# Kernel tuning notes

Hardware: AMD Instinct MI355X
Metric: run time of the kernel (lower is better)

The kernel has to match this reference:

```python
import jax, jax.numpy as jnp
import numpy as np

NUM_HEADS = 16
NUM_HIDDENS = 1024
NEG_INF = -1e6


def setup_inputs() -> dict:
    key = jax.random.key(0)
    ks = jax.random.split(key, 8)
    B, S, D = 2, 2048, NUM_HIDDENS
    scale = 1.0 / np.sqrt(D)
    return {
        "q": jax.random.normal(ks[0], (B, S, D), jnp.float32),
        "k": jax.random.normal(ks[1], (B, S, D), jnp.float32),
        "v": jax.random.normal(ks[2], (B, S, D), jnp.float32),
        # nn.Linear weights have shape (out_features, in_features)
        "Wq": jax.random.normal(ks[3], (D, D), jnp.float32) * scale,
        "Wk": jax.random.normal(ks[4], (D, D), jnp.float32) * scale,
        "Wv": jax.random.normal(ks[5], (D, D), jnp.float32) * scale,
        "Wo": jax.random.normal(ks[6], (D, D), jnp.float32) * scale,
        "valid_len": jax.random.randint(ks[7], (B,), 1, 2048 + 1, jnp.int32),
    }


def _unpack_heads(x, nh):
    # (B, S, H) -> (B*nh, S, H//nh), matching Unpack_base_head
    B, S, H = x.shape
    return x.reshape(B, S, nh, H // nh).transpose(0, 2, 1, 3).reshape(B * nh, S, H // nh)


def _merge_heads(x, nh):
    # Faithful to Merge_base_head: (B*nh, S, dh) -> (B, nh, S, dh)
    # -> permute(0,2,3,1) -> (B, S, dh, nh) -> (B, S, dh*nh)
    Bnh, S, dh = x.shape
    B = Bnh // nh
    x = x.reshape(B, nh, S, dh).transpose(0, 2, 3, 1)
    return x.reshape(B, S, dh * nh)


def reference(q, k, v, Wq, Wk, Wv, Wo, valid_len):
    nh = NUM_HEADS
    # projections (bias=False); Linear: x @ W.T
    qh = _unpack_heads(q @ Wq.T, nh)  # (B*nh, S, dh)
    kh = _unpack_heads(k @ Wk.T, nh)
    vh = _unpack_heads(v @ Wv.T, nh)
    dh = qh.shape[-1]
    scores = jnp.einsum("bqd,bkd->bqk", qh, kh) / jnp.sqrt(jnp.float32(dh))
    # repeat_interleave valid_len by num_heads along dim 0
    vl = jnp.repeat(valid_len, nh)  # (B*nh,)
    key_pos = jnp.arange(scores.shape[-1])  # (S,)
    mask = key_pos[None, None, :] < vl[:, None, None]  # (B*nh, 1, S)
    scores = jnp.where(mask, scores, NEG_INF)
    attn = jax.nn.softmax(scores, axis=-1)  # dropout=0.0 (eval) -> identity
    out = jnp.einsum("bqk,bkd->bqd", attn, vh)  # (B*nh, S, dh)
    out = _merge_heads(out, nh) @ Wo.T  # (B, S, H)
    return out, attn
```

## Files before the change

### kernel.cpp

```cpp
#include <hip/hip_runtime.h>
#include <stdint.h>

#define SB 2048
#define DB 1024
#define NHB 16
#define DHB 64

typedef __attribute__((ext_vector_type(8))) short short8;
typedef __attribute__((ext_vector_type(4))) short short4v;
typedef __attribute__((ext_vector_type(4))) float f32x4;

#define SC2 0.18033688011112042f

__device__ __forceinline__ unsigned short f2bf(float f) {
  union { float f; uint32_t u; } v; v.f = f;
  uint32_t u = v.u;
  return (unsigned short)((u + 0x7FFFu + ((u >> 16) & 1u)) >> 16);
}

__device__ __forceinline__ void gld16(const void* g, void* l) {
  __builtin_amdgcn_global_load_lds(
      (const __attribute__((address_space(1))) void*)g,
      (__attribute__((address_space(3))) void*)l, 16, 0, 0);
}

__device__ __forceinline__ int xcd_swz(int bid, int nwg) {
  return (bid & 7) * (nwg >> 3) + (bid >> 3);
}

struct ConvArgs {
  const float* s[7];
  unsigned short* d[7];
  int n[7];
};

__global__ __launch_bounds__(256) void conv_kernel(ConvArgs a) {
  const int t = blockIdx.y;
  const float* __restrict__ src = a.s[t];
  unsigned short* __restrict__ dst = a.d[t];
  const int n8 = a.n[t] >> 3;
  for (int i = blockIdx.x * 256 + threadIdx.x; i < n8; i += gridDim.x * 256) {
    const f32x4* p = (const f32x4*)src + (size_t)i * 2;
    f32x4 x = p[0], y = p[1];
    short8 o;
    o[0] = (short)f2bf(x[0]); o[1] = (short)f2bf(x[1]);
    o[2] = (short)f2bf(x[2]); o[3] = (short)f2bf(x[3]);
    o[4] = (short)f2bf(y[0]); o[5] = (short)f2bf(y[1]);
    o[6] = (short)f2bf(y[2]); o[7] = (short)f2bf(y[3]);
    *(short8*)(dst + (size_t)i * 8) = o;
  }
}

struct GemmArgs {
  const unsigned short* A[3];
  const unsigned short* B[3];
  void* O[3];
  int mode[3];
};

__global__ __launch_bounds__(256) void gemm128(GemmArgs ga, const int* __restrict__ vlen,
                                               float* __restrict__ attn_out) {
  __shared__ unsigned short SH[17408];

  if (blockIdx.x >= 256) {
    const int NF = 258;
    const int fid = blockIdx.y * 86 + (blockIdx.x - 256);
    f32x4 z;
    z[0] = 0.f; z[1] = 0.f; z[2] = 0.f; z[3] = 0.f;
    const int vls[2] = {vlen[0], vlen[1]};
    for (int rw = fid; rw < 32 * SB; rw += NF) {
      int bh = rw >> 11, row = rw & 2047;
      int vl = vls[bh >> 4];
      int c0 = min(32, (vl + 63) >> 6) * 64;
      float* dst = attn_out + (size_t)bh * SB * SB + (size_t)row * SB;
      for (int c4 = (c0 >> 2) + threadIdx.x; c4 < (SB >> 2); c4 += 256)
        __builtin_nontemporal_store(z, (f32x4*)dst + c4);
    }
    return;
  }

  unsigned short* Ab = SH;
  unsigned short* Bb = SH + 8192;

  const int z = blockIdx.y;
  const unsigned short* __restrict__ A = ga.A[z];
  const unsigned short* __restrict__ Bw = ga.B[z];
  const int mode = ga.mode[z];

  const int tid = threadIdx.x;
  const int w = tid >> 6, lane = tid & 63;
  const int g = lane >> 4, li = lane & 15;
  const int wm = w >> 1, wn = w & 1;
  const int l = xcd_swz(blockIdx.x, 256);
  const int m0 = (l >> 3) * 128, n0 = (l & 7) * 128;

  const int srow = lane >> 3;
  const int sg = (lane & 7) ^ srow;

  f32x4 acc[4][4];
  #pragma unroll
  for (int i = 0; i < 4; ++i)
    #pragma unroll
    for (int j = 0; j < 4; ++j)
      #pragma unroll
      for (int e = 0; e < 4; ++e) acc[i][j][e] = 0.f;

  for (int k0 = 0; k0 < DB; k0 += 64) {
    __syncthreads();
    #pragma unroll
    for (int i = 0; i < 4; ++i) {
      int c = w * 4 + i;
      gld16(A + (size_t)(m0 + c * 8 + srow) * DB + k0 + sg * 8, Ab + c * 512);
      gld16(Bw + (size_t)(n0 + c * 8 + srow) * DB + k0 + sg * 8, Bb + c * 512);
    }
    __syncthreads();
    short8 af[4][2], bf[4][2];
    #pragma unroll
    for (int mf = 0; mf < 4; ++mf)
      #pragma unroll
      for (int ks = 0; ks < 2; ++ks)
        af[mf][ks] = *(const short8*)&Ab[(wm * 64 + mf * 16 + li) * 64 +
                                         (((ks * 4 + g) ^ (li & 7)) << 3)];
    #pragma unroll
    for (int nf = 0; nf < 4; ++nf)
      #pragma unroll
      for (int ks = 0; ks < 2; ++ks)
        bf[nf][ks] = *(const short8*)&Bb[(wn * 64 + nf * 16 + li) * 64 +
                                         (((ks * 4 + g) ^ (li & 7)) << 3)];
    __builtin_amdgcn_s_setprio(1);
    #pragma unroll
    for (int ks = 0; ks < 2; ++ks)
      #pragma unroll
      for (int mf = 0; mf < 4; ++mf)
        #pragma unroll
        for (int nf = 0; nf < 4; ++nf)
          acc[mf][nf] = __builtin_amdgcn_mfma_f32_16x16x32_bf16(
              af[mf][ks], bf[nf][ks], acc[mf][nf], 0, 0, 0);
    __builtin_amdgcn_s_setprio(0);
  }

  if (mode == 0) {
    unsigned short* O = (unsigned short*)ga.O[z];
    #pragma unroll
    for (int mf = 0; mf < 4; ++mf)
      #pragma unroll
      for (int nf = 0; nf < 4; ++nf)
        #pragma unroll
        for (int r = 0; r < 4; ++r) {
          int row = m0 + wm * 64 + mf * 16 + g * 4 + r;
          int col = n0 + wn * 64 + nf * 16 + li;
          int b_ = row >> 11, s_ = row & 2047;
          int h = col >> 6, dp = col & 63;
          O[((size_t)(b_ * NHB + h) * SB + s_) * DHB + dp] = f2bf(acc[mf][nf][r]);
        }
  } else {
    unsigned short* O = (unsigned short*)ga.O[z];
    __syncthreads();
    #pragma unroll
    for (int mf = 0; mf < 4; ++mf)
      #pragma unroll
      for (int nf = 0; nf < 4; ++nf) {
        short4v pk;
        #pragma unroll
        for (int r = 0; r < 4; ++r) pk[r] = (short)f2bf(acc[mf][nf][r]);
        *(short4v*)&SH[(size_t)(wn * 64 + nf * 16 + li) * 136 +
                       wm * 64 + mf * 16 + g * 4] = pk;
      }
    __syncthreads();
    int c = tid >> 1, rh = tid & 1;
    int col = n0 + c;
    int h = col >> 6, dp = col & 63;
    int b_ = m0 >> 11, s0 = (m0 & 2047) + rh * 64;
    unsigned short* dst = O + ((size_t)(b_ * NHB + h) * DHB + dp) * SB + s0;
    #pragma unroll
    for (int j = 0; j < 8; ++j)
      *(short8*)(dst + j * 8) = *(const short8*)&SH[c * 136 + rh * 64 + j * 8];
  }
}

__global__ __launch_bounds__(256) void attn_kernel(
    const unsigned short* __restrict__ Qh, const unsigned short* __restrict__ Kh,
    const unsigned short* __restrict__ Vt, const int* __restrict__ valid_len,
    float* __restrict__ attn_out, unsigned short* __restrict__ Mg)
{
  __shared__ unsigned short Kb[2][4096];
  __shared__ unsigned short Vb[2][4096];
  __shared__ unsigned short QP[128][88];

  const int tid = threadIdx.x;
  const int wave = tid >> 6, lane = tid & 63;
  const int g = lane >> 4, li = lane & 15;
  const int lsw = xcd_swz(blockIdx.x, 512);
  const int q0 = (lsw & 15) * 128;
  const int bh = lsw >> 4;
  const int b_ = bh >> 4;
  const int vl = valid_len[b_];
  const int nkt = min(32, (vl + 63) >> 6);

  const int srow = lane >> 3;
  const int sg = (lane & 7) ^ srow;

  {
    int qr = tid >> 1, half = (tid & 1) * 32;
    const unsigned short* src = Qh + ((size_t)bh * SB + q0 + qr) * DHB + half;
    #pragma unroll
    for (int j = 0; j < 4; ++j)
      *(short8*)&QP[qr][half + j * 8] = *(const short8*)(src + j * 8);
  }
  __syncthreads();

  short8 qa[2][2];
  #pragma unroll
  for (int qf = 0; qf < 2; ++qf)
    #pragma unroll
    for (int ks = 0; ks < 2; ++ks)
      qa[qf][ks] = *(const short8*)&QP[wave * 32 + qf * 16 + li][ks * 32 + g * 8];

  float lQ[2] = {0.f, 0.f};

  {
    #pragma unroll
    for (int i = 0; i < 2; ++i) {
      int c = wave * 2 + i;
      gld16(Kh + ((size_t)bh * SB + 0 + c * 8 + srow) * DHB + sg * 8,
            &Kb[0][c * 512]);
    }
    int cur = 0;
    for (int kti = 0; kti < nkt; ++kti) {
      const int kt = kti * 64;
      __syncthreads();
      if (kti + 1 < nkt) {
        #pragma unroll
        for (int i = 0; i < 2; ++i) {
          int c = wave * 2 + i;
          gld16(Kh + ((size_t)bh * SB + kt + 64 + c * 8 + srow) * DHB + sg * 8,
                &Kb[cur ^ 1][c * 512]);
        }
      }
      f32x4 sc[2][4];
      #pragma unroll
      for (int qf = 0; qf < 2; ++qf)
        #pragma unroll
        for (int nf = 0; nf < 4; ++nf)
          #pragma unroll
          for (int j = 0; j < 4; ++j) sc[qf][nf][j] = 0.f;
      __builtin_amdgcn_s_setprio(1);
      #pragma unroll
      for (int ks = 0; ks < 2; ++ks)
        #pragma unroll
        for (int nf = 0; nf < 4; ++nf) {
          short8 kbf = *(const short8*)&Kb[cur][(nf * 16 + li) * 64 +
                                               (((ks * 4 + g) ^ (li & 7)) << 3)];
          #pragma unroll
          for (int qf = 0; qf < 2; ++qf)
            sc[qf][nf] = __builtin_amdgcn_mfma_f32_16x16x32_bf16(
                kbf, qa[qf][ks], sc[qf][nf], 0, 0, 0);
        }
      __builtin_amdgcn_s_setprio(0);
      #pragma unroll
      for (int qf = 0; qf < 2; ++qf) {
        float la = 0.f;
        #pragma unroll
        for (int nf = 0; nf < 4; ++nf)
          #pragma unroll
          for (int r = 0; r < 4; ++r) {
            int key = kt + nf * 16 + g * 4 + r;
            float s2 = (key < vl) ? sc[qf][nf][r] * SC2 : -1.5e6f;
            la += exp2f(s2);
          }
        lQ[qf] += la;
      }
      cur ^= 1;
    }
  }
  __syncthreads();

  float rlQ[2];
  #pragma unroll
  for (int qf = 0; qf < 2; ++qf) {
    float L = lQ[qf];
    L += __shfl_xor(L, 16);
    L += __shfl_xor(L, 32);
    rlQ[qf] = 1.f / L;
  }

  f32x4 oacc[2][4];
  #pragma unroll
  for (int qf = 0; qf < 2; ++qf)
    #pragma unroll
    for (int nf = 0; nf < 4; ++nf)
      #pragma unroll
      for (int j = 0; j < 4; ++j) oacc[qf][nf][j] = 0.f;

  {
    #pragma unroll
    for (int i = 0; i < 2; ++i) {
      int c = wave * 2 + i;
      gld16(Kh + ((size_t)bh * SB + c * 8 + srow) * DHB + sg * 8, &Kb[0][c * 512]);
      gld16(Vt + ((size_t)bh * DHB + c * 8 + srow) * SB + 0 + sg * 8, &Vb[0][c * 512]);
    }
    int cur = 0;
    for (int kti = 0; kti < nkt; ++kti) {
      const int kt = kti * 64;
      __syncthreads();
      if (kti + 1 < nkt) {
        #pragma unroll
        for (int i = 0; i < 2; ++i) {
          int c = wave * 2 + i;
          gld16(Kh + ((size_t)bh * SB + kt + 64 + c * 8 + srow) * DHB + sg * 8,
                &Kb[cur ^ 1][c * 512]);
          gld16(Vt + ((size_t)bh * DHB + c * 8 + srow) * SB + kt + 64 + sg * 8,
                &Vb[cur ^ 1][c * 512]);
        }
      }
      f32x4 sc[2][4];
      #pragma unroll
      for (int qf = 0; qf < 2; ++qf)
        #pragma unroll
        for (int nf = 0; nf < 4; ++nf)
          #pragma unroll
          for (int j = 0; j < 4; ++j) sc[qf][nf][j] = 0.f;
      __builtin_amdgcn_s_setprio(1);
      #pragma unroll
      for (int ks = 0; ks < 2; ++ks)
        #pragma unroll
        for (int nf = 0; nf < 4; ++nf) {
          short8 kbf = *(const short8*)&Kb[cur][(nf * 16 + li) * 64 +
                                               (((ks * 4 + g) ^ (li & 7)) << 3)];
          #pragma unroll
          for (int qf = 0; qf < 2; ++qf)
            sc[qf][nf] = __builtin_amdgcn_mfma_f32_16x16x32_bf16(
                kbf, qa[qf][ks], sc[qf][nf], 0, 0, 0);
        }
      __builtin_amdgcn_s_setprio(0);
      #pragma unroll
      for (int qf = 0; qf < 2; ++qf) {
        int qrow = q0 + wave * 32 + qf * 16 + li;
        #pragma unroll
        for (int nf = 0; nf < 4; ++nf) {
          short4v pk;
          #pragma unroll
          for (int r = 0; r < 4; ++r) {
            int key = kt + nf * 16 + g * 4 + r;
            float s2 = (key < vl) ? sc[qf][nf][r] * SC2 : -1.5e6f;
            float p = exp2f(s2) * rlQ[qf];
            sc[qf][nf][r] = p;
            pk[r] = (short)f2bf(p);
          }
          __builtin_nontemporal_store(
              sc[qf][nf],
              (f32x4*)(attn_out + (size_t)bh * SB * SB + (size_t)qrow * SB +
                       kt + nf * 16 + g * 4));
          *(short4v*)&QP[wave * 32 + qf * 16 + li][nf * 16 + g * 4] = pk;
        }
      }
      __builtin_amdgcn_s_setprio(1);
      #pragma unroll
      for (int ks = 0; ks < 2; ++ks) {
        short8 vbf[4];
        #pragma unroll
        for (int nf = 0; nf < 4; ++nf)
          vbf[nf] = *(const short8*)&Vb[cur][(nf * 16 + li) * 64 +
                                             (((ks * 4 + g) ^ (li & 7)) << 3)];
        #pragma unroll
        for (int qf = 0; qf < 2; ++qf) {
          short8 pa = *(const short8*)&QP[wave * 32 + qf * 16 + li][ks * 32 + g * 8];
          #pragma unroll
          for (int nf = 0; nf < 4; ++nf)
            oacc[qf][nf] = __builtin_amdgcn_mfma_f32_16x16x32_bf16(
                pa, vbf[nf], oacc[qf][nf], 0, 0, 0);
        }
      }
      __builtin_amdgcn_s_setprio(0);
      cur ^= 1;
    }
  }

  const int h = bh & 15;
  #pragma unroll
  for (int qf = 0; qf < 2; ++qf)
    #pragma unroll
    for (int nf = 0; nf < 4; ++nf)
      #pragma unroll
      for (int r = 0; r < 4; ++r) {
        int qrow = q0 + wave * 32 + qf * 16 + g * 4 + r;
        int dp = nf * 16 + li;
        Mg[((size_t)b_ * SB + qrow) * DB + dp * NHB + h] = f2bf(oacc[qf][nf][r]);
      }
}

__global__ __launch_bounds__(256) void outproj_kernel(
    const unsigned short* __restrict__ A, const unsigned short* __restrict__ Bw,
    float* __restrict__ Out)
{
  __shared__ unsigned short SH[12288];
  unsigned short* Ab = SH;
  unsigned short* Bb = SH + 8192;

  const int tid = threadIdx.x;
  const int w = tid >> 6, lane = tid & 63;
  const int g = lane >> 4, li = lane & 15;
  const int wm = w >> 1, wn = w & 1;
  const int l = xcd_swz(blockIdx.x, 512);
  const int m0 = (l >> 4) * 128, n0 = (l & 15) * 64;

  const int srow = lane >> 3;
  const int sg = (lane & 7) ^ srow;

  int a_off[4][2], b_off[2][2];
  #pragma unroll
  for (int mf = 0; mf < 4; ++mf) {
    int row = wm * 64 + mf * 16 + li;
    #pragma unroll
    for (int ks = 0; ks < 2; ++ks)
      a_off[mf][ks] = row * 64 + (((ks * 4 + g) ^ (li & 7)) << 3);
  }
  #pragma unroll
  for (int nf = 0; nf < 2; ++nf) {
    int row = wn * 32 + nf * 16 + li;
    #pragma unroll
    for (int ks = 0; ks < 2; ++ks)
      b_off[nf][ks] = row * 64 + (((ks * 4 + g) ^ (li & 7)) << 3);
  }

  f32x4 acc[4][2];
  #pragma unroll
  for (int i = 0; i < 4; ++i)
    #pragma unroll
    for (int j = 0; j < 2; ++j)
      #pragma unroll
      for (int e = 0; e < 4; ++e) acc[i][j][e] = 0.f;

  for (int k0 = 0; k0 < DB; k0 += 64) {
    __syncthreads();
    #pragma unroll
    for (int i = 0; i < 4; ++i) {
      int c = w * 4 + i;
      gld16(A + (size_t)(m0 + c * 8 + srow) * DB + k0 + sg * 8, Ab + c * 512);
    }
    #pragma unroll
    for (int i = 0; i < 2; ++i) {
      int c = w * 2 + i;
      gld16(Bw + (size_t)(n0 + c * 8 + srow) * DB + k0 + sg * 8, Bb + c * 512);
    }
    __syncthreads();
    short8 af[4][2], bf[2][2];
    #pragma unroll
    for (int mf = 0; mf < 4; ++mf)
      #pragma unroll
      for (int ks = 0; ks < 2; ++ks)
        af[mf][ks] = *(const short8*)&Ab[a_off[mf][ks]];
    #pragma unroll
    for (int nf = 0; nf < 2; ++nf)
      #pragma unroll
      for (int ks = 0; ks < 2; ++ks)
        bf[nf][ks] = *(const short8*)&Bb[b_off[nf][ks]];
    __builtin_amdgcn_s_setprio(1);
    #pragma unroll
    for (int ks = 0; ks < 2; ++ks)
      #pragma unroll
      for (int mf = 0; mf < 4; ++mf)
        #pragma unroll
        for (int nf = 0; nf < 2; ++nf)
          acc[mf][nf] = __builtin_amdgcn_mfma_f32_16x16x32_bf16(
              af[mf][ks], bf[nf][ks], acc[mf][nf], 0, 0, 0);
    __builtin_amdgcn_s_setprio(0);
  }

  #pragma unroll
  for (int mf = 0; mf < 4; ++mf)
    #pragma unroll
    for (int nf = 0; nf < 2; ++nf)
      #pragma unroll
      for (int r = 0; r < 4; ++r) {
        int row = m0 + wm * 64 + mf * 16 + g * 4 + r;
        int col = n0 + wn * 32 + nf * 16 + li;
        Out[(size_t)row * DB + col] = acc[mf][nf][r];
      }
}

extern "C" void kernel_launch(void* const* d_in, const int* in_sizes, int n_in,
                              void* d_out, int out_size, void* d_ws, size_t ws_size,
                              hipStream_t stream) {
  const float* q  = (const float*)d_in[0];
  const float* k  = (const float*)d_in[1];
  const float* v  = (const float*)d_in[2];
  const float* Wq = (const float*)d_in[3];
  const float* Wk = (const float*)d_in[4];
  const float* Wv = (const float*)d_in[5];
  const float* Wo = (const float*)d_in[6];
  const int* vlen = (const int*)d_in[7];

  const size_t HS = (size_t)2 * NHB * SB * DHB;
  const size_t WS = (size_t)DB * DB;

  unsigned short* ws = (unsigned short*)d_ws;
  unsigned short* qb  = ws;
  unsigned short* kb  = qb + HS;
  unsigned short* vb  = kb + HS;
  unsigned short* Wqb = vb + HS;
  unsigned short* Wkb = Wqb + WS;
  unsigned short* Wvb = Wkb + WS;
  unsigned short* Wob = Wvb + WS;
  unsigned short* Qh  = Wob + WS;
  unsigned short* Kh  = Qh + HS;
  unsigned short* Vt  = Kh + HS;
  unsigned short* Mg  = qb;

  float* out  = (float*)d_out;
  float* attn = out + (size_t)2 * SB * DB;

  ConvArgs ca;
  ca.s[0] = q;  ca.d[0] = qb;  ca.n[0] = (int)HS;
  ca.s[1] = k;  ca.d[1] = kb;  ca.n[1] = (int)HS;
  ca.s[2] = v;  ca.d[2] = vb;  ca.n[2] = (int)HS;
  ca.s[3] = Wq; ca.d[3] = Wqb; ca.n[3] = (int)WS;
  ca.s[4] = Wk; ca.d[4] = Wkb; ca.n[4] = (int)WS;
  ca.s[5] = Wv; ca.d[5] = Wvb; ca.n[5] = (int)WS;
  ca.s[6] = Wo; ca.d[6] = Wob; ca.n[6] = (int)WS;

  GemmArgs pa;
  pa.A[0] = qb;  pa.A[1] = kb;  pa.A[2] = vb;
  pa.B[0] = Wqb; pa.B[1] = Wkb; pa.B[2] = Wvb;
  pa.O[0] = Qh;  pa.O[1] = Kh;  pa.O[2] = Vt;
  pa.mode[0] = 0; pa.mode[1] = 0; pa.mode[2] = 1;

  dim3 blk(256);
  conv_kernel<<<dim3(1024, 7), blk, 0, stream>>>(ca);
  gemm128<<<dim3(342, 3), blk, 0, stream>>>(pa, vlen, attn);
  attn_kernel<<<dim3(512), blk, 0, stream>>>(Qh, Kh, Vt, vlen, attn, Mg);
  outproj_kernel<<<dim3(512), blk, 0, stream>>>(Mg, Wob, out);
}
```

Measured before the change: 258.4 us.

## Move attn zero-fill into attention kernel and coalesce merged-head stores

Several changes land together. The zeroing of masked attention columns moves out of the projection GEMM's extra blocks into the tail of the attention kernel. The attention output goes through shared memory so it can be written as contiguous head slices. To make that valid, Wo is permuted during bf16 conversion so the output projection sees a head-contiguous merged layout. Q fragments are now loaded straight from global memory, fully valid key tiles skip the mask check, and the block-to-head mapping is remapped per XCD for cache locality. The risk is that the attention kernel now carries the large zero-fill writes itself, and the strided Wo conversion is slower than the vectorised path.

```diff
diff --git a/kernel.cpp b/kernel.cpp
--- a/kernel.cpp
+++ b/kernel.cpp
@@ -29,13 +29,23 @@
 }
 
 struct ConvArgs {
-  const float* s[7];
-  unsigned short* d[7];
-  int n[7];
+  const float* s[6];
+  unsigned short* d[6];
+  int n[6];
 };
 
-__global__ __launch_bounds__(256) void conv_kernel(ConvArgs a) {
+__global__ __launch_bounds__(256) void conv_kernel(ConvArgs a,
+                                                   const float* __restrict__ Wo,
+                                                   unsigned short* __restrict__ Wob) {
   const int t = blockIdx.y;
+  if (t == 6) {
+    for (int i = blockIdx.x * 256 + threadIdx.x; i < DB * DB; i += gridDim.x * 256) {
+      int o = i >> 10, cp = i & 1023;
+      int src = (o << 10) + ((cp & 63) << 4) + (cp >> 6);
+      Wob[i] = f2bf(Wo[src]);
+    }
+    return;
+  }
   const float* __restrict__ src = a.s[t];
   unsigned short* __restrict__ dst = a.d[t];
   const int n8 = a.n[t] >> 3;
@@ -58,27 +68,8 @@
   int mode[3];
 };
 
-__global__ __launch_bounds__(256) void gemm128(GemmArgs ga, const int* __restrict__ vlen,
-                                               float* __restrict__ attn_out) {
+__global__ __launch_bounds__(256) void gemm128(GemmArgs ga) {
   __shared__ unsigned short SH[17408];
-
-  if (blockIdx.x >= 256) {
-    const int NF = 258;
-    const int fid = blockIdx.y * 86 + (blockIdx.x - 256);
-    f32x4 z;
-    z[0] = 0.f; z[1] = 0.f; z[2] = 0.f; z[3] = 0.f;
-    const int vls[2] = {vlen[0], vlen[1]};
-    for (int rw = fid; rw < 32 * SB; rw += NF) {
-      int bh = rw >> 11, row = rw & 2047;
-      int vl = vls[bh >> 4];
-      int c0 = min(32, (vl + 63) >> 6) * 64;
-      float* dst = attn_out + (size_t)bh * SB * SB + (size_t)row * SB;
-      for (int c4 = (c0 >> 2) + threadIdx.x; c4 < (SB >> 2); c4 += 256)
-        __builtin_nontemporal_store(z, (f32x4*)dst + c4);
-    }
-    return;
-  }
-
   unsigned short* Ab = SH;
   unsigned short* Bb = SH + 8192;
 
@@ -185,14 +176,15 @@
 {
   __shared__ unsigned short Kb[2][4096];
   __shared__ unsigned short Vb[2][4096];
-  __shared__ unsigned short QP[128][88];
+  __shared__ unsigned short P[128][72];
 
   const int tid = threadIdx.x;
   const int wave = tid >> 6, lane = tid & 63;
   const int g = lane >> 4, li = lane & 15;
   const int lsw = xcd_swz(blockIdx.x, 512);
-  const int q0 = (lsw & 15) * 128;
-  const int bh = lsw >> 4;
+  const int xcd = lsw >> 6, j = lsw & 63;
+  const int bh = ((j >> 5) << 4) + xcd * 2 + ((j >> 4) & 1);
+  const int q0 = (j & 15) * 128;
   const int b_ = bh >> 4;
   const int vl = valid_len[b_];
   const int nkt = min(32, (vl + 63) >> 6);
@@ -200,50 +192,43 @@
   const int srow = lane >> 3;
   const int sg = (lane & 7) ^ srow;
 
+  const size_t kbase = (size_t)bh * SB * DHB;
+  const size_t vbase = (size_t)bh * DHB * SB;
+
+  short8 qa[2][2];
+  #pragma unroll
+  for (int qf = 0; qf < 2; ++qf)
+    #pragma unroll
+    for (int ks = 0; ks < 2; ++ks)
+      qa[qf][ks] = *(const short8*)(
+          Qh + ((size_t)bh * SB + q0 + wave * 32 + qf * 16 + li) * DHB +
+          ks * 32 + g * 8);
+
+  float lQ[2] = {0.f, 0.f};
+
   {
-    int qr = tid >> 1, half = (tid & 1) * 32;
-    const unsigned short* src = Qh + ((size_t)bh * SB + q0 + qr) * DHB + half;
-    #pragma unroll
-    for (int j = 0; j < 4; ++j)
-      *(short8*)&QP[qr][half + j * 8] = *(const short8*)(src + j * 8);
-  }
-  __syncthreads();
-
-  short8 qa[2][2];
-  #pragma unroll
-  for (int qf = 0; qf < 2; ++qf)
-    #pragma unroll
-    for (int ks = 0; ks < 2; ++ks)
-      qa[qf][ks] = *(const short8*)&QP[wave * 32 + qf * 16 + li][ks * 32 + g * 8];
-
-  float lQ[2] = {0.f, 0.f};
-
-  {
-    #pragma unroll
-    for (int i = 0; i < 2; ++i) {
-      int c = wave * 2 + i;
-      gld16(Kh + ((size_t)bh * SB + 0 + c * 8 + srow) * DHB + sg * 8,
-            &Kb[0][c * 512]);
-    }
+    const int c = wave * 2;
+    gld16(Kh + kbase + (size_t)(c * 8 + srow) * DHB + sg * 8, &Kb[0][c * 512]);
+    gld16(Kh + kbase + (size_t)((c + 1) * 8 + srow) * DHB + sg * 8,
+          &Kb[0][(c + 1) * 512]);
     int cur = 0;
     for (int kti = 0; kti < nkt; ++kti) {
-      const int kt = kti * 64;
       __syncthreads();
       if (kti + 1 < nkt) {
-        #pragma unroll
-        for (int i = 0; i < 2; ++i) {
-          int c = wave * 2 + i;
-          gld16(Kh + ((size_t)bh * SB + kt + 64 + c * 8 + srow) * DHB + sg * 8,
-                &Kb[cur ^ 1][c * 512]);
-        }
-      }
+        int kn = (kti + 1) * 64;
+        gld16(Kh + kbase + (size_t)(kn + c * 8 + srow) * DHB + sg * 8,
+              &Kb[cur ^ 1][c * 512]);
+        gld16(Kh + kbase + (size_t)(kn + (c + 1) * 8 + srow) * DHB + sg * 8,
+              &Kb[cur ^ 1][(c + 1) * 512]);
+      }
+      const int kt = kti * 64;
       f32x4 sc[2][4];
       #pragma unroll
       for (int qf = 0; qf < 2; ++qf)
         #pragma unroll
         for (int nf = 0; nf < 4; ++nf)
           #pragma unroll
-          for (int j = 0; j < 4; ++j) sc[qf][nf][j] = 0.f;
+          for (int e = 0; e < 4; ++e) sc[qf][nf][e] = 0.f;
       __builtin_amdgcn_s_setprio(1);
       #pragma unroll
       for (int ks = 0; ks < 2; ++ks)
@@ -257,18 +242,30 @@
                 kbf, qa[qf][ks], sc[qf][nf], 0, 0, 0);
         }
       __builtin_amdgcn_s_setprio(0);
-      #pragma unroll
-      for (int qf = 0; qf < 2; ++qf) {
-        float la = 0.f;
-        #pragma unroll
-        for (int nf = 0; nf < 4; ++nf)
-          #pragma unroll
-          for (int r = 0; r < 4; ++r) {
-            int key = kt + nf * 16 + g * 4 + r;
-            float s2 = (key < vl) ? sc[qf][nf][r] * SC2 : -1.5e6f;
-            la += exp2f(s2);
-          }
-        lQ[qf] += la;
+      if (kt + 64 <= vl) {
+        #pragma unroll
+        for (int qf = 0; qf < 2; ++qf) {
+          float la = 0.f;
+          #pragma unroll
+          for (int nf = 0; nf < 4; ++nf)
+            #pragma unroll
+            for (int r = 0; r < 4; ++r) la += exp2f(sc[qf][nf][r] * SC2);
+          lQ[qf] += la;
+        }
+      } else {
+        #pragma unroll
+        for (int qf = 0; qf < 2; ++qf) {
+          float la = 0.f;
+          #pragma unroll
+          for (int nf = 0; nf < 4; ++nf)
+            #pragma unroll
+            for (int r = 0; r < 4; ++r) {
+              int key = kt + nf * 16 + g * 4 + r;
+              float s2 = (key < vl) ? sc[qf][nf][r] * SC2 : -1.5e6f;
+              la += exp2f(s2);
+            }
+          lQ[qf] += la;
+        }
       }
       cur ^= 1;
     }
@@ -290,36 +287,38 @@
     #pragma unroll
     for (int nf = 0; nf < 4; ++nf)
       #pragma unroll
-      for (int j = 0; j < 4; ++j) oacc[qf][nf][j] = 0.f;
+      for (int e = 0; e < 4; ++e) oacc[qf][nf][e] = 0.f;
 
   {
-    #pragma unroll
-    for (int i = 0; i < 2; ++i) {
-      int c = wave * 2 + i;
-      gld16(Kh + ((size_t)bh * SB + c * 8 + srow) * DHB + sg * 8, &Kb[0][c * 512]);
-      gld16(Vt + ((size_t)bh * DHB + c * 8 + srow) * SB + 0 + sg * 8, &Vb[0][c * 512]);
-    }
+    const int c = wave * 2;
+    gld16(Kh + kbase + (size_t)(c * 8 + srow) * DHB + sg * 8, &Kb[0][c * 512]);
+    gld16(Kh + kbase + (size_t)((c + 1) * 8 + srow) * DHB + sg * 8,
+          &Kb[0][(c + 1) * 512]);
+    gld16(Vt + vbase + (size_t)(c * 8 + srow) * SB + sg * 8, &Vb[0][c * 512]);
+    gld16(Vt + vbase + (size_t)((c + 1) * 8 + srow) * SB + sg * 8,
+          &Vb[0][(c + 1) * 512]);
     int cur = 0;
     for (int kti = 0; kti < nkt; ++kti) {
-      const int kt = kti * 64;
       __syncthreads();
       if (kti + 1 < nkt) {
-        #pragma unroll
-        for (int i = 0; i < 2; ++i) {
-          int c = wave * 2 + i;
-          gld16(Kh + ((size_t)bh * SB + kt + 64 + c * 8 + srow) * DHB + sg * 8,
-                &Kb[cur ^ 1][c * 512]);
-          gld16(Vt + ((size_t)bh * DHB + c * 8 + srow) * SB + kt + 64 + sg * 8,
-                &Vb[cur ^ 1][c * 512]);
-        }
-      }
+        int kn = (kti + 1) * 64;
+        gld16(Kh + kbase + (size_t)(kn + c * 8 + srow) * DHB + sg * 8,
+              &Kb[cur ^ 1][c * 512]);
+        gld16(Kh + kbase + (size_t)(kn + (c + 1) * 8 + srow) * DHB + sg * 8,
+              &Kb[cur ^ 1][(c + 1) * 512]);
+        gld16(Vt + vbase + (size_t)(c * 8 + srow) * SB + kn + sg * 8,
+              &Vb[cur ^ 1][c * 512]);
+        gld16(Vt + vbase + (size_t)((c + 1) * 8 + srow) * SB + kn + sg * 8,
+              &Vb[cur ^ 1][(c + 1) * 512]);
+      }
+      const int kt = kti * 64;
       f32x4 sc[2][4];
       #pragma unroll
       for (int qf = 0; qf < 2; ++qf)
         #pragma unroll
         for (int nf = 0; nf < 4; ++nf)
           #pragma unroll
-          for (int j = 0; j < 4; ++j) sc[qf][nf][j] = 0.f;
+          for (int e = 0; e < 4; ++e) sc[qf][nf][e] = 0.f;
       __builtin_amdgcn_s_setprio(1);
       #pragma unroll
       for (int ks = 0; ks < 2; ++ks)
@@ -333,25 +332,35 @@
                 kbf, qa[qf][ks], sc[qf][nf], 0, 0, 0);
         }
       __builtin_amdgcn_s_setprio(0);
+      const bool fullt = (kt + 64 <= vl);
       #pragma unroll
       for (int qf = 0; qf < 2; ++qf) {
-        int qrow = q0 + wave * 32 + qf * 16 + li;
+        const int qrow = q0 + wave * 32 + qf * 16 + li;
         #pragma unroll
         for (int nf = 0; nf < 4; ++nf) {
           short4v pk;
-          #pragma unroll
-          for (int r = 0; r < 4; ++r) {
-            int key = kt + nf * 16 + g * 4 + r;
-            float s2 = (key < vl) ? sc[qf][nf][r] * SC2 : -1.5e6f;
-            float p = exp2f(s2) * rlQ[qf];
-            sc[qf][nf][r] = p;
-            pk[r] = (short)f2bf(p);
+          if (fullt) {
+            #pragma unroll
+            for (int r = 0; r < 4; ++r) {
+              float p = exp2f(sc[qf][nf][r] * SC2) * rlQ[qf];
+              sc[qf][nf][r] = p;
+              pk[r] = (short)f2bf(p);
+            }
+          } else {
+            #pragma unroll
+            for (int r = 0; r < 4; ++r) {
+              int key = kt + nf * 16 + g * 4 + r;
+              float s2 = (key < vl) ? sc[qf][nf][r] * SC2 : -1.5e6f;
+              float p = exp2f(s2) * rlQ[qf];
+              sc[qf][nf][r] = p;
+              pk[r] = (short)f2bf(p);
+            }
           }
           __builtin_nontemporal_store(
               sc[qf][nf],
               (f32x4*)(attn_out + (size_t)bh * SB * SB + (size_t)qrow * SB +
                        kt + nf * 16 + g * 4));
-          *(short4v*)&QP[wave * 32 + qf * 16 + li][nf * 16 + g * 4] = pk;
+          *(short4v*)&P[wave * 32 + qf * 16 + li][nf * 16 + g * 4] = pk;
         }
       }
       __builtin_amdgcn_s_setprio(1);
@@ -361,10 +370,10 @@
         #pragma unroll
         for (int nf = 0; nf < 4; ++nf)
           vbf[nf] = *(const short8*)&Vb[cur][(nf * 16 + li) * 64 +
-                                             (((ks * 4 + g) ^ (li & 7)) << 3)];
+                                            (((ks * 4 + g) ^ (li & 7)) << 3)];
         #pragma unroll
         for (int qf = 0; qf < 2; ++qf) {
-          short8 pa = *(const short8*)&QP[wave * 32 + qf * 16 + li][ks * 32 + g * 8];
+          short8 pa = *(const short8*)&P[wave * 32 + qf * 16 + li][ks * 32 + g * 8];
           #pragma unroll
           for (int nf = 0; nf < 4; ++nf)
             oacc[qf][nf] = __builtin_amdgcn_mfma_f32_16x16x32_bf16(
@@ -376,17 +385,37 @@
     }
   }
 
+  {
+    int c0 = nkt * 64;
+    int rem4 = (SB - c0) >> 2;
+    if (rem4 > 0) {
+      f32x4 z;
+      z[0] = 0.f; z[1] = 0.f; z[2] = 0.f; z[3] = 0.f;
+      for (int row = 0; row < 128; ++row) {
+        float* dst = attn_out + (size_t)bh * SB * SB + (size_t)(q0 + row) * SB + c0;
+        for (int c = tid; c < rem4; c += 256)
+          __builtin_nontemporal_store(z, (f32x4*)dst + c);
+      }
+    }
+  }
+
+  __syncthreads();
   const int h = bh & 15;
   #pragma unroll
   for (int qf = 0; qf < 2; ++qf)
     #pragma unroll
     for (int nf = 0; nf < 4; ++nf)
       #pragma unroll
-      for (int r = 0; r < 4; ++r) {
-        int qrow = q0 + wave * 32 + qf * 16 + g * 4 + r;
-        int dp = nf * 16 + li;
-        Mg[((size_t)b_ * SB + qrow) * DB + dp * NHB + h] = f2bf(oacc[qf][nf][r]);
-      }
+      for (int r = 0; r < 4; ++r)
+        P[wave * 32 + qf * 16 + g * 4 + r][nf * 16 + li] = f2bf(oacc[qf][nf][r]);
+  __syncthreads();
+  {
+    int row = tid >> 1, half = (tid & 1) * 32;
+    unsigned short* dst = Mg + ((size_t)b_ * SB + q0 + row) * DB + h * 64 + half;
+    #pragma unroll
+    for (int j2 = 0; j2 < 4; ++j2)
+      *(short8*)(dst + j2 * 8) = *(const short8*)&P[row][half + j2 * 8];
+  }
 }
 
 __global__ __launch_bounds__(256) void outproj_kernel(
@@ -517,7 +546,6 @@
   ca.s[3] = Wq; ca.d[3] = Wqb; ca.n[3] = (int)WS;
   ca.s[4] = Wk; ca.d[4] = Wkb; ca.n[4] = (int)WS;
   ca.s[5] = Wv; ca.d[5] = Wvb; ca.n[5] = (int)WS;
-  ca.s[6] = Wo; ca.d[6] = Wob; ca.n[6] = (int)WS;
 
   GemmArgs pa;
   pa.A[0] = qb;  pa.A[1] = kb;  pa.A[2] = vb;
@@ -526,8 +554,8 @@
   pa.mode[0] = 0; pa.mode[1] = 0; pa.mode[2] = 1;
 
   dim3 blk(256);
-  conv_kernel<<<dim3(1024, 7), blk, 0, stream>>>(ca);
-  gemm128<<<dim3(342, 3), blk, 0, stream>>>(pa, vlen, attn);
+  conv_kernel<<<dim3(1024, 7), blk, 0, stream>>>(ca, Wo, Wob);
+  gemm128<<<dim3(256, 3), blk, 0, stream>>>(pa);
   attn_kernel<<<dim3(512), blk, 0, stream>>>(Qh, Kh, Vt, vlen, attn, Mg);
   outproj_kernel<<<dim3(512), blk, 0, stream>>>(Mg, Wob, out);
 }
```

After: 223.2 us. -13.6%, faster.
